# Kernel optimization log

Hardware: AMD Instinct MI355X
Metric: run time of the kernel (lower is better)

Reference implementation:

```python
import jax, jax.numpy as jnp
import numpy as np

B, A, T, D = 8, 50, 256, 128
HEADS, C = 32, 4  # C = D // HEADS
NEG_SLOPE = 0.2   # PyG GATConv default negative_slope


def setup_inputs() -> dict:
    key = jax.random.key(0)
    k1, k2, k3, k4 = jax.random.split(key, 4)
    h = jax.random.normal(k1, (B, A, T, D), dtype=jnp.float32)
    # PyG Linear weight [heads*out, in], applied as x @ W.T
    W = jax.random.normal(k2, (HEADS * C, D), dtype=jnp.float32) * (1.0 / np.sqrt(D))
    att_src = jax.random.normal(k3, (HEADS, C), dtype=jnp.float32) * 0.1
    att_dst = jax.random.normal(k4, (HEADS, C), dtype=jnp.float32) * 0.1
    bias = jnp.zeros((HEADS * C,), dtype=jnp.float32)
    return {"h": h, "W": W, "att_src": att_src, "att_dst": att_dst, "bias": bias}


def reference(h, W, att_src, att_dst, bias):
    # Graph is fully-connected-minus-self over A agents, replicated B*T times.
    # Equivalent dense form: per-destination softmax over all sources j != i.
    Bv, Av, Tv, Dv = h.shape
    x = h.transpose(0, 2, 1, 3).reshape(Bv * Tv, Av, Dv)          # [N, A, D], N = B*T graphs
    x = jnp.einsum('nad,ed->nae', x, W).reshape(Bv * Tv, Av, HEADS, C)  # W x, per head
    a_src = jnp.einsum('nahc,hc->nah', x, att_src)                # alpha_src[j]
    a_dst = jnp.einsum('nahc,hc->nah', x, att_dst)                # alpha_dst[i]
    # edge (j -> i): e_ij = leaky_relu(alpha_src[j] + alpha_dst[i])
    e = a_dst[:, :, None, :] + a_src[:, None, :, :]               # [N, i, j, H]
    e = jnp.where(e > 0, e, NEG_SLOPE * e)
    diag = jnp.eye(Av, dtype=bool)[None, :, :, None]              # no self-loops
    e = jnp.where(diag, -jnp.inf, e)
    alpha = jax.nn.softmax(e, axis=2)                             # scatter-softmax over src per dst
    out = jnp.einsum('nijh,njhc->nihc', alpha, x)                 # scatter-add aggregation
    out = out.reshape(Bv * Tv, Av, HEADS * C) + bias              # concat heads + bias
    return out.reshape(Bv, Tv, Av, HEADS * C).transpose(0, 2, 1, 3)  # (B, A, T, D)
```

## Files before the change

### kernel.cpp

```cpp
#include <hip/hip_runtime.h>
#include <hip/hip_bf16.h>

#define LOG2E 1.4426950408889634f

typedef __attribute__((ext_vector_type(8))) short bf16x8;
typedef __attribute__((ext_vector_type(4))) float f32x4;
typedef __attribute__((ext_vector_type(2))) float v2f;

static __device__ __forceinline__ float fast_exp2(float x) {
    return __builtin_amdgcn_exp2f(x);
}

static __device__ __forceinline__ short bf16bits(float f) {
    __hip_bfloat16 b = __float2bfloat16(f);
    return *reinterpret_cast<short*>(&b);
}

__global__ void wconv(const float* __restrict__ W, short* __restrict__ Wb) {
    const int i = blockIdx.x * 256 + threadIdx.x;
    Wb[i] = bf16bits(W[i]);
}

template<bool PRE>
__global__ __launch_bounds__(256, 3) void gat_fused(
    const float* __restrict__ hsrc,
    const float* __restrict__ W,
    const short* __restrict__ Wb,
    const float* __restrict__ att_src,
    const float* __restrict__ att_dst,
    const float* __restrict__ bias,
    float* __restrict__ out)
{
    constexpr int A = 50, T = 256, D = 128, H = 32;
    constexpr int XSS = 132;
    __shared__ __align__(16) char smem[25600 + A * XSS * 4];
    v2f*   EsFs = (v2f*)smem;
    v2f*   EdFd = (v2f*)(smem + 12800);
    short* hsb  = (short*)smem;
    float* xs   = (float*)(smem + 25600);

    const int n = blockIdx.x;
    const int b = n >> 8;
    const int t = n & 255;
    const int tid = threadIdx.x;

    const float4* hg4 = (const float4*)hsrc;
    for (int idx = tid; idx < 64 * 32; idx += 256) {
        const int a = idx >> 5, k4 = idx & 31;
        short4 pk = {0, 0, 0, 0};
        if (a < A) {
            const float4 hv = hg4[((size_t)(b * A + a) * T + t) * 32 + k4];
            pk.x = bf16bits(hv.x); pk.y = bf16bits(hv.y);
            pk.z = bf16bits(hv.z); pk.w = bf16bits(hv.w);
        }
        const int swz = (k4 >> 1) ^ (a & 7);
        *(short4*)&hsb[a * 128 + swz * 8 + (k4 & 1) * 4] = pk;
    }
    __syncthreads();

    {
        const int wv = tid >> 6;
        const int lane = tid & 63;
        const int lr = lane & 15, lg = lane >> 4;
        const int n0 = wv * 32;
        f32x4 acc[4][2];
        #pragma unroll
        for (int m = 0; m < 4; ++m) {
            acc[m][0] = (f32x4){0.f, 0.f, 0.f, 0.f};
            acc[m][1] = (f32x4){0.f, 0.f, 0.f, 0.f};
        }
        #pragma unroll
        for (int kk = 0; kk < 4; ++kk) {
            bf16x8 bf0, bf1;
            if (PRE) {
                const bf16x8* Wb8 = (const bf16x8*)Wb;
                bf0 = Wb8[(size_t)(n0 + lr) * 16 + kk * 4 + lg];
                bf1 = Wb8[(size_t)(n0 + 16 + lr) * 16 + kk * 4 + lg];
            } else {
                const float4* W4 = (const float4*)W;
                const int kb = kk * 8 + lg * 2;
                const float4 wa = W4[(size_t)(n0 + lr) * 32 + kb];
                const float4 wb = W4[(size_t)(n0 + lr) * 32 + kb + 1];
                const float4 wc = W4[(size_t)(n0 + 16 + lr) * 32 + kb];
                const float4 wd = W4[(size_t)(n0 + 16 + lr) * 32 + kb + 1];
                bf0[0] = bf16bits(wa.x); bf0[1] = bf16bits(wa.y);
                bf0[2] = bf16bits(wa.z); bf0[3] = bf16bits(wa.w);
                bf0[4] = bf16bits(wb.x); bf0[5] = bf16bits(wb.y);
                bf0[6] = bf16bits(wb.z); bf0[7] = bf16bits(wb.w);
                bf1[0] = bf16bits(wc.x); bf1[1] = bf16bits(wc.y);
                bf1[2] = bf16bits(wc.z); bf1[3] = bf16bits(wc.w);
                bf1[4] = bf16bits(wd.x); bf1[5] = bf16bits(wd.y);
                bf1[6] = bf16bits(wd.z); bf1[7] = bf16bits(wd.w);
            }
            #pragma unroll
            for (int m = 0; m < 4; ++m) {
                const int row = m * 16 + lr;
                const int chunk = (kk * 4 + lg) ^ (row & 7);
                const bf16x8 af = *(const bf16x8*)&hsb[row * 128 + chunk * 8];
                acc[m][0] = __builtin_amdgcn_mfma_f32_16x16x32_bf16(af, bf0, acc[m][0], 0, 0, 0);
                acc[m][1] = __builtin_amdgcn_mfma_f32_16x16x32_bf16(af, bf1, acc[m][1], 0, 0, 0);
            }
        }
        #pragma unroll
        for (int m = 0; m < 4; ++m) {
            const int rb = m * 16 + lg * 4;
            #pragma unroll
            for (int nt = 0; nt < 2; ++nt) {
                const int col = n0 + nt * 16 + lr;
                #pragma unroll
                for (int r = 0; r < 4; ++r) {
                    if (rb + r < A) xs[(rb + r) * XSS + col] = acc[m][nt][r];
                }
            }
        }
    }
    __syncthreads();

    for (int idx = tid; idx < A * H; idx += 256) {
        const int hh = idx & 31, a = idx >> 5;
        const float4 xv = *(const float4*)&xs[a * XSS + hh * 4];
        const float4 s4 = ((const float4*)att_src)[hh];
        const float4 d4 = ((const float4*)att_dst)[hh];
        const float asc = LOG2E * fmaf(xv.w, s4.w, fmaf(xv.z, s4.z, fmaf(xv.y, s4.y, xv.x * s4.x)));
        const float ads = LOG2E * fmaf(xv.w, d4.w, fmaf(xv.z, d4.z, fmaf(xv.y, d4.y, xv.x * d4.x)));
        EsFs[idx] = (v2f){fast_exp2(asc), fast_exp2(0.2f * asc)};
        EdFd[idx] = (v2f){fast_exp2(ads), fast_exp2(0.2f * ads)};
    }
    __syncthreads();

    {
        const int hh = tid & 31;
        const int ib = tid >> 5;
        v2f acc01[7], acc23[7], df[7];
        float l[7];
        #pragma unroll
        for (int r = 0; r < 7; ++r) {
            const int i = ib + 8 * r;
            const int ii = (i < A) ? i : (A - 1);
            df[r] = EdFd[ii * H + hh];
            acc01[r] = (v2f){0.f, 0.f};
            acc23[r] = (v2f){0.f, 0.f};
            l[r] = 0.f;
        }
        #pragma unroll 5
        for (int j = 0; j < A; ++j) {
            const v2f sf = EsFs[j * H + hh];
            const float4 xv = *(const float4*)&xs[j * XSS + hh * 4];
            const v2f x01 = (v2f){xv.x, xv.y};
            const v2f x23 = (v2f){xv.z, xv.w};
            #pragma unroll
            for (int r = 0; r < 7; ++r) {
                const v2f pe = df[r] * sf;
                const float p = fmaxf(pe.x, pe.y);
                l[r] += p;
                const v2f pp = (v2f){p, p};
                acc01[r] = __builtin_elementwise_fma(pp, x01, acc01[r]);
                acc23[r] = __builtin_elementwise_fma(pp, x23, acc23[r]);
            }
        }
        const float4 bv = ((const float4*)bias)[hh];
        #pragma unroll
        for (int r = 0; r < 7; ++r) {
            const int i = ib + 8 * r;
            if (i < A) {
                const v2f sf = EsFs[i * H + hh];
                const float4 xv = *(const float4*)&xs[i * XSS + hh * 4];
                const v2f pe = df[r] * sf;
                const float p = fmaxf(pe.x, pe.y);
                const float linv = 1.0f / (l[r] - p);
                float4 o;
                o.x = fmaf(acc01[r].x - p * xv.x, linv, bv.x);
                o.y = fmaf(acc01[r].y - p * xv.y, linv, bv.y);
                o.z = fmaf(acc23[r].x - p * xv.z, linv, bv.z);
                o.w = fmaf(acc23[r].y - p * xv.w, linv, bv.w);
                *(float4*)&out[((size_t)(b * A + i) * T + t) * D + hh * 4] = o;
            }
        }
    }
}

extern "C" void kernel_launch(void* const* d_in, const int* in_sizes, int n_in,
                              void* d_out, int out_size, void* d_ws, size_t ws_size,
                              hipStream_t stream) {
    const float* h       = (const float*)d_in[0];
    const float* W       = (const float*)d_in[1];
    const float* att_src = (const float*)d_in[2];
    const float* att_dst = (const float*)d_in[3];
    const float* bias    = (const float*)d_in[4];
    float* out = (float*)d_out;
    dim3 grid(8 * 256);
    dim3 block(256);
    if (ws_size >= 128 * 128 * sizeof(short)) {
        short* Wb = (short*)d_ws;
        hipLaunchKernelGGL(wconv, dim3(64), block, 0, stream, W, Wb);
        hipLaunchKernelGGL(gat_fused<true>, grid, block, 0, stream,
                           h, W, Wb, att_src, att_dst, bias, out);
    } else {
        hipLaunchKernelGGL(gat_fused<false>, grid, block, 0, stream,
                           h, W, (const short*)nullptr, att_src, att_dst, bias, out);
    }
}
```

Measured before the change: 57.75 us.

## Move attention aggregation onto bf16 MFMA with transposed bf16 projection storage

Replaces the scalar per-thread attention aggregation with a bf16 MFMA. Attention weights are built as the A operand, and the projected features are stored transposed in bf16 in LDS as the B operand. An extra all-ones column computes the softmax denominator inside the same MFMA. Shared memory drops and the launch-bounds occupancy target rises from 3 to 4. The cost is two head phases with extra syncs, rounding of x and the weights to bf16, and a scattered scalar output store of one float per lane.

```diff
diff --git a/kernel.cpp b/kernel.cpp
--- a/kernel.cpp
+++ b/kernel.cpp
@@ -10,11 +10,14 @@
 static __device__ __forceinline__ float fast_exp2(float x) {
     return __builtin_amdgcn_exp2f(x);
 }
-
 static __device__ __forceinline__ short bf16bits(float f) {
     __hip_bfloat16 b = __float2bfloat16(f);
     return *reinterpret_cast<short*>(&b);
 }
+static __device__ __forceinline__ unsigned packbf(float lo, float hi) {
+    return (unsigned)(unsigned short)bf16bits(lo)
+         | ((unsigned)(unsigned short)bf16bits(hi) << 16);
+}
 
 __global__ void wconv(const float* __restrict__ W, short* __restrict__ Wb) {
     const int i = blockIdx.x * 256 + threadIdx.x;
@@ -22,7 +25,7 @@
 }
 
 template<bool PRE>
-__global__ __launch_bounds__(256, 3) void gat_fused(
+__global__ __launch_bounds__(256, 4) void gat_fused(
     const float* __restrict__ hsrc,
     const float* __restrict__ W,
     const short* __restrict__ Wb,
@@ -31,18 +34,20 @@
     const float* __restrict__ bias,
     float* __restrict__ out)
 {
-    constexpr int A = 50, T = 256, D = 128, H = 32;
-    constexpr int XSS = 132;
-    __shared__ __align__(16) char smem[25600 + A * XSS * 4];
-    v2f*   EsFs = (v2f*)smem;
-    v2f*   EdFd = (v2f*)(smem + 12800);
+    constexpr int A = 50, T = 256, D = 128;
+    constexpr int XJ = 72;
+    __shared__ __align__(16) char smem[16384 + 129 * XJ * 2];
+    float* esfs = (float*)smem;
+    float* edfd = (float*)(smem + 8192);
+    short* xsT  = (short*)(smem + 16384);
     short* hsb  = (short*)smem;
-    float* xs   = (float*)(smem + 25600);
 
     const int n = blockIdx.x;
     const int b = n >> 8;
     const int t = n & 255;
     const int tid = threadIdx.x;
+    const int lane = tid & 63, lr = lane & 15, lg = lane >> 4;
+    const int w = tid >> 6;
 
     const float4* hg4 = (const float4*)hsrc;
     for (int idx = tid; idx < 64 * 32; idx += 256) {
@@ -56,13 +61,11 @@
         const int swz = (k4 >> 1) ^ (a & 7);
         *(short4*)&hsb[a * 128 + swz * 8 + (k4 & 1) * 4] = pk;
     }
+    if (tid < 64) xsT[128 * XJ + tid] = (short)0x3F80;
     __syncthreads();
 
     {
-        const int wv = tid >> 6;
-        const int lane = tid & 63;
-        const int lr = lane & 15, lg = lane >> 4;
-        const int n0 = wv * 32;
+        const int n0 = w * 32;
         f32x4 acc[4][2];
         #pragma unroll
         for (int m = 0; m < 4; ++m) {
@@ -103,79 +106,110 @@
         }
         #pragma unroll
         for (int m = 0; m < 4; ++m) {
-            const int rb = m * 16 + lg * 4;
+            const int row0 = m * 16 + lg * 4;
             #pragma unroll
             for (int nt = 0; nt < 2; ++nt) {
                 const int col = n0 + nt * 16 + lr;
+                const unsigned w0 = packbf(acc[m][nt][0], acc[m][nt][1]);
+                const unsigned w1 = packbf(acc[m][nt][2], acc[m][nt][3]);
+                *(uint2*)&xsT[col * XJ + row0] = (uint2){w0, w1};
+            }
+        }
+    }
+    __syncthreads();
+
+    const float4* as4 = (const float4*)att_src;
+    const float4* ad4 = (const float4*)att_dst;
+
+    #pragma unroll 1
+    for (int ph = 0; ph < 2; ++ph) {
+        #pragma unroll
+        for (int p = 0; p < 4; ++p) {
+            const int idx = p * 256 + tid;
+            const int hl = idx >> 6, a = idx & 63;
+            v2f sf = (v2f){0.f, 0.f}, df = (v2f){0.f, 0.f};
+            if (a < A) {
+                const int hg = ph * 16 + hl;
+                const int cb = (hg * 4) * XJ + a;
+                const float x0 = __uint_as_float((unsigned)(unsigned short)xsT[cb] << 16);
+                const float x1 = __uint_as_float((unsigned)(unsigned short)xsT[cb + XJ] << 16);
+                const float x2 = __uint_as_float((unsigned)(unsigned short)xsT[cb + 2 * XJ] << 16);
+                const float x3 = __uint_as_float((unsigned)(unsigned short)xsT[cb + 3 * XJ] << 16);
+                const float4 s4 = as4[hg], d4 = ad4[hg];
+                const float as = LOG2E * fmaf(x3, s4.w, fmaf(x2, s4.z, fmaf(x1, s4.y, x0 * s4.x)));
+                const float ad = LOG2E * fmaf(x3, d4.w, fmaf(x2, d4.z, fmaf(x1, d4.y, x0 * d4.x)));
+                sf = (v2f){fast_exp2(as), fast_exp2(0.2f * as)};
+                df = (v2f){fast_exp2(ad), fast_exp2(0.2f * ad)};
+            }
+            *(v2f*)&esfs[idx * 2] = sf;
+            *(v2f*)&edfd[idx * 2] = df;
+        }
+        __syncthreads();
+
+        #pragma unroll 1
+        for (int u = 0; u < 4; ++u) {
+            const int hl = w * 4 + u;
+            const int hg = ph * 16 + hl;
+            const int colmap = (lr < 4) ? (hg * 4 + lr) : 128;
+            f32x4 acc[4];
+            #pragma unroll
+            for (int m = 0; m < 4; ++m) acc[m] = (f32x4){0.f, 0.f, 0.f, 0.f};
+            #pragma unroll
+            for (int kt = 0; kt < 2; ++kt) {
+                const int k0 = kt * 32;
+                const int j0 = k0 + lg * 8;
+                const float4* ep = (const float4*)&esfs[(hl * 64 + j0) * 2];
+                const float4 e0 = ep[0], e1 = ep[1], e2 = ep[2], e3 = ep[3];
+                union { uint4 q; bf16x8 v; } bfr;
+                bfr.q = *(const uint4*)&xsT[colmap * XJ + j0];
+                #pragma unroll
+                for (int m = 0; m < 4; ++m) {
+                    const int row = m * 16 + lr;
+                    const v2f dd = *(const v2f*)&edfd[(hl * 64 + row) * 2];
+                    float p0 = fmaxf(dd.x * e0.x, dd.y * e0.y);
+                    float p1 = fmaxf(dd.x * e0.z, dd.y * e0.w);
+                    float p2 = fmaxf(dd.x * e1.x, dd.y * e1.y);
+                    float p3 = fmaxf(dd.x * e1.z, dd.y * e1.w);
+                    float p4 = fmaxf(dd.x * e2.x, dd.y * e2.y);
+                    float p5 = fmaxf(dd.x * e2.z, dd.y * e2.w);
+                    float p6 = fmaxf(dd.x * e3.x, dd.y * e3.y);
+                    float p7 = fmaxf(dd.x * e3.z, dd.y * e3.w);
+                    const int dm = m * 16 - k0;
+                    if (dm >= -15 && dm <= 23) {
+                        const int dq = row - j0;
+                        p0 = (dq == 0) ? 0.f : p0;
+                        p1 = (dq == 1) ? 0.f : p1;
+                        p2 = (dq == 2) ? 0.f : p2;
+                        p3 = (dq == 3) ? 0.f : p3;
+                        p4 = (dq == 4) ? 0.f : p4;
+                        p5 = (dq == 5) ? 0.f : p5;
+                        p6 = (dq == 6) ? 0.f : p6;
+                        p7 = (dq == 7) ? 0.f : p7;
+                    }
+                    union { unsigned uu[4]; bf16x8 v; } afr;
+                    afr.uu[0] = packbf(p0, p1);
+                    afr.uu[1] = packbf(p2, p3);
+                    afr.uu[2] = packbf(p4, p5);
+                    afr.uu[3] = packbf(p6, p7);
+                    acc[m] = __builtin_amdgcn_mfma_f32_16x16x32_bf16(afr.v, bfr.v, acc[m], 0, 0, 0);
+                }
+            }
+            const float bv = bias[hg * 4 + (lr & 3)];
+            #pragma unroll
+            for (int m = 0; m < 4; ++m) {
                 #pragma unroll
                 for (int r = 0; r < 4; ++r) {
-                    if (rb + r < A) xs[(rb + r) * XSS + col] = acc[m][nt][r];
+                    const float lsum = __shfl(acc[m][r], (lane & 48) | 4, 64);
+                    const int row = m * 16 + lg * 4 + r;
+                    if (lr < 4 && row < A) {
+                        const float linv = __builtin_amdgcn_rcpf(fmaxf(lsum, 1e-20f));
+                        const float o = fmaf(acc[m][r], linv, bv);
+                        out[((size_t)(b * A + row) * T + t) * D + hg * 4 + lr] = o;
+                    }
                 }
             }
         }
-    }
-    __syncthreads();
-
-    for (int idx = tid; idx < A * H; idx += 256) {
-        const int hh = idx & 31, a = idx >> 5;
-        const float4 xv = *(const float4*)&xs[a * XSS + hh * 4];
-        const float4 s4 = ((const float4*)att_src)[hh];
-        const float4 d4 = ((const float4*)att_dst)[hh];
-        const float asc = LOG2E * fmaf(xv.w, s4.w, fmaf(xv.z, s4.z, fmaf(xv.y, s4.y, xv.x * s4.x)));
-        const float ads = LOG2E * fmaf(xv.w, d4.w, fmaf(xv.z, d4.z, fmaf(xv.y, d4.y, xv.x * d4.x)));
-        EsFs[idx] = (v2f){fast_exp2(asc), fast_exp2(0.2f * asc)};
-        EdFd[idx] = (v2f){fast_exp2(ads), fast_exp2(0.2f * ads)};
-    }
-    __syncthreads();
-
-    {
-        const int hh = tid & 31;
-        const int ib = tid >> 5;
-        v2f acc01[7], acc23[7], df[7];
-        float l[7];
-        #pragma unroll
-        for (int r = 0; r < 7; ++r) {
-            const int i = ib + 8 * r;
-            const int ii = (i < A) ? i : (A - 1);
-            df[r] = EdFd[ii * H + hh];
-            acc01[r] = (v2f){0.f, 0.f};
-            acc23[r] = (v2f){0.f, 0.f};
-            l[r] = 0.f;
-        }
-        #pragma unroll 5
-        for (int j = 0; j < A; ++j) {
-            const v2f sf = EsFs[j * H + hh];
-            const float4 xv = *(const float4*)&xs[j * XSS + hh * 4];
-            const v2f x01 = (v2f){xv.x, xv.y};
-            const v2f x23 = (v2f){xv.z, xv.w};
-            #pragma unroll
-            for (int r = 0; r < 7; ++r) {
-                const v2f pe = df[r] * sf;
-                const float p = fmaxf(pe.x, pe.y);
-                l[r] += p;
-                const v2f pp = (v2f){p, p};
-                acc01[r] = __builtin_elementwise_fma(pp, x01, acc01[r]);
-                acc23[r] = __builtin_elementwise_fma(pp, x23, acc23[r]);
-            }
-        }
-        const float4 bv = ((const float4*)bias)[hh];
-        #pragma unroll
-        for (int r = 0; r < 7; ++r) {
-            const int i = ib + 8 * r;
-            if (i < A) {
-                const v2f sf = EsFs[i * H + hh];
-                const float4 xv = *(const float4*)&xs[i * XSS + hh * 4];
-                const v2f pe = df[r] * sf;
-                const float p = fmaxf(pe.x, pe.y);
-                const float linv = 1.0f / (l[r] - p);
-                float4 o;
-                o.x = fmaf(acc01[r].x - p * xv.x, linv, bv.x);
-                o.y = fmaf(acc01[r].y - p * xv.y, linv, bv.y);
-                o.z = fmaf(acc23[r].x - p * xv.z, linv, bv.z);
-                o.w = fmaf(acc23[r].y - p * xv.w, linv, bv.w);
-                *(float4*)&out[((size_t)(b * A + i) * T + t) * D + hh * 4] = o;
-            }
-        }
+        __syncthreads();
     }
 }
 
```

Result: slower. 93.77 us (+62.4%).

## Split each graph's heads across two blocks to raise occupancy

Applied to the files above, without the earlier changes.

Each graph is now processed by two blocks, each handling 16 of the 32 heads (64 output columns). This halves the shared memory per block and the per-thread register arrays, and launch bounds rise to 6 blocks per CU. The cost is that each block still loads and converts the full h tile to bf16, so global reads of h double and the small GEMM's row tiling is redone per block. A barrier is added before xs is written because xs is no longer separate from the h staging buffer.

```diff
diff --git a/kernel.cpp b/kernel.cpp
--- a/kernel.cpp
+++ b/kernel.cpp
@@ -10,7 +10,6 @@
 static __device__ __forceinline__ float fast_exp2(float x) {
     return __builtin_amdgcn_exp2f(x);
 }
-
 static __device__ __forceinline__ short bf16bits(float f) {
     __hip_bfloat16 b = __float2bfloat16(f);
     return *reinterpret_cast<short*>(&b);
@@ -22,7 +21,7 @@
 }
 
 template<bool PRE>
-__global__ __launch_bounds__(256, 3) void gat_fused(
+__global__ __launch_bounds__(256, 6) void gat_fused(
     const float* __restrict__ hsrc,
     const float* __restrict__ W,
     const short* __restrict__ Wb,
@@ -31,18 +30,22 @@
     const float* __restrict__ bias,
     float* __restrict__ out)
 {
-    constexpr int A = 50, T = 256, D = 128, H = 32;
-    constexpr int XSS = 132;
-    __shared__ __align__(16) char smem[25600 + A * XSS * 4];
-    v2f*   EsFs = (v2f*)smem;
-    v2f*   EdFd = (v2f*)(smem + 12800);
+    constexpr int A = 50, T = 256, D = 128;
+    constexpr int XC = 68;
+    __shared__ __align__(16) char smem[12800 + A * XC * 4];
+    v2f*   tabS = (v2f*)smem;
+    v2f*   tabD = (v2f*)(smem + 6400);
+    float* xs   = (float*)(smem + 12800);
     short* hsb  = (short*)smem;
-    float* xs   = (float*)(smem + 25600);
 
-    const int n = blockIdx.x;
+    const int bid = blockIdx.x;
+    const int n = bid >> 1;
+    const int hp = bid & 1;
     const int b = n >> 8;
     const int t = n & 255;
     const int tid = threadIdx.x;
+    const int lane = tid & 63, lr = lane & 15, lg = lane >> 4;
+    const int wv = tid >> 6;
 
     const float4* hg4 = (const float4*)hsrc;
     for (int idx = tid; idx < 64 * 32; idx += 256) {
@@ -59,97 +62,85 @@
     __syncthreads();
 
     {
-        const int wv = tid >> 6;
-        const int lane = tid & 63;
-        const int lr = lane & 15, lg = lane >> 4;
-        const int n0 = wv * 32;
-        f32x4 acc[4][2];
+        const int rbase = wv * 16;
+        f32x4 acc[4];
         #pragma unroll
-        for (int m = 0; m < 4; ++m) {
-            acc[m][0] = (f32x4){0.f, 0.f, 0.f, 0.f};
-            acc[m][1] = (f32x4){0.f, 0.f, 0.f, 0.f};
-        }
+        for (int nt = 0; nt < 4; ++nt) acc[nt] = (f32x4){0.f, 0.f, 0.f, 0.f};
         #pragma unroll
         for (int kk = 0; kk < 4; ++kk) {
-            bf16x8 bf0, bf1;
-            if (PRE) {
-                const bf16x8* Wb8 = (const bf16x8*)Wb;
-                bf0 = Wb8[(size_t)(n0 + lr) * 16 + kk * 4 + lg];
-                bf1 = Wb8[(size_t)(n0 + 16 + lr) * 16 + kk * 4 + lg];
-            } else {
-                const float4* W4 = (const float4*)W;
-                const int kb = kk * 8 + lg * 2;
-                const float4 wa = W4[(size_t)(n0 + lr) * 32 + kb];
-                const float4 wb = W4[(size_t)(n0 + lr) * 32 + kb + 1];
-                const float4 wc = W4[(size_t)(n0 + 16 + lr) * 32 + kb];
-                const float4 wd = W4[(size_t)(n0 + 16 + lr) * 32 + kb + 1];
-                bf0[0] = bf16bits(wa.x); bf0[1] = bf16bits(wa.y);
-                bf0[2] = bf16bits(wa.z); bf0[3] = bf16bits(wa.w);
-                bf0[4] = bf16bits(wb.x); bf0[5] = bf16bits(wb.y);
-                bf0[6] = bf16bits(wb.z); bf0[7] = bf16bits(wb.w);
-                bf1[0] = bf16bits(wc.x); bf1[1] = bf16bits(wc.y);
-                bf1[2] = bf16bits(wc.z); bf1[3] = bf16bits(wc.w);
-                bf1[4] = bf16bits(wd.x); bf1[5] = bf16bits(wd.y);
-                bf1[6] = bf16bits(wd.z); bf1[7] = bf16bits(wd.w);
-            }
+            const int row = rbase + lr;
+            const int chunk = (kk * 4 + lg) ^ (row & 7);
+            const bf16x8 af = *(const bf16x8*)&hsb[row * 128 + chunk * 8];
             #pragma unroll
-            for (int m = 0; m < 4; ++m) {
-                const int row = m * 16 + lr;
-                const int chunk = (kk * 4 + lg) ^ (row & 7);
-                const bf16x8 af = *(const bf16x8*)&hsb[row * 128 + chunk * 8];
-                acc[m][0] = __builtin_amdgcn_mfma_f32_16x16x32_bf16(af, bf0, acc[m][0], 0, 0, 0);
-                acc[m][1] = __builtin_amdgcn_mfma_f32_16x16x32_bf16(af, bf1, acc[m][1], 0, 0, 0);
+            for (int nt = 0; nt < 4; ++nt) {
+                const int e = hp * 64 + nt * 16 + lr;
+                bf16x8 bf;
+                if (PRE) {
+                    bf = ((const bf16x8*)Wb)[(size_t)e * 16 + kk * 4 + lg];
+                } else {
+                    const float4* W4 = (const float4*)W;
+                    const int kb = kk * 8 + lg * 2;
+                    const float4 wa = W4[(size_t)e * 32 + kb];
+                    const float4 wb = W4[(size_t)e * 32 + kb + 1];
+                    bf[0] = bf16bits(wa.x); bf[1] = bf16bits(wa.y);
+                    bf[2] = bf16bits(wa.z); bf[3] = bf16bits(wa.w);
+                    bf[4] = bf16bits(wb.x); bf[5] = bf16bits(wb.y);
+                    bf[6] = bf16bits(wb.z); bf[7] = bf16bits(wb.w);
+                }
+                acc[nt] = __builtin_amdgcn_mfma_f32_16x16x32_bf16(af, bf, acc[nt], 0, 0, 0);
             }
         }
+        __syncthreads();
         #pragma unroll
-        for (int m = 0; m < 4; ++m) {
-            const int rb = m * 16 + lg * 4;
+        for (int nt = 0; nt < 4; ++nt) {
             #pragma unroll
-            for (int nt = 0; nt < 2; ++nt) {
-                const int col = n0 + nt * 16 + lr;
-                #pragma unroll
-                for (int r = 0; r < 4; ++r) {
-                    if (rb + r < A) xs[(rb + r) * XSS + col] = acc[m][nt][r];
-                }
+            for (int r = 0; r < 4; ++r) {
+                const int row = rbase + lg * 4 + r;
+                if (row < A) xs[row * XC + nt * 16 + lr] = acc[nt][r];
             }
         }
     }
     __syncthreads();
 
-    for (int idx = tid; idx < A * H; idx += 256) {
-        const int hh = idx & 31, a = idx >> 5;
-        const float4 xv = *(const float4*)&xs[a * XSS + hh * 4];
-        const float4 s4 = ((const float4*)att_src)[hh];
-        const float4 d4 = ((const float4*)att_dst)[hh];
-        const float asc = LOG2E * fmaf(xv.w, s4.w, fmaf(xv.z, s4.z, fmaf(xv.y, s4.y, xv.x * s4.x)));
-        const float ads = LOG2E * fmaf(xv.w, d4.w, fmaf(xv.z, d4.z, fmaf(xv.y, d4.y, xv.x * d4.x)));
-        EsFs[idx] = (v2f){fast_exp2(asc), fast_exp2(0.2f * asc)};
-        EdFd[idx] = (v2f){fast_exp2(ads), fast_exp2(0.2f * ads)};
+    for (int p = 0; p < 4; ++p) {
+        const int idx = p * 256 + tid;
+        if (idx < A * 16) {
+            const int a = idx >> 4, hl = idx & 15;
+            const int hg = hp * 16 + hl;
+            const float4 xv = *(const float4*)&xs[a * XC + hl * 4];
+            const float4 s4 = ((const float4*)att_src)[hg];
+            const float4 d4 = ((const float4*)att_dst)[hg];
+            const float asc = LOG2E * fmaf(xv.w, s4.w, fmaf(xv.z, s4.z, fmaf(xv.y, s4.y, xv.x * s4.x)));
+            const float ads = LOG2E * fmaf(xv.w, d4.w, fmaf(xv.z, d4.z, fmaf(xv.y, d4.y, xv.x * d4.x)));
+            tabS[idx] = (v2f){fast_exp2(asc), fast_exp2(0.2f * asc)};
+            tabD[idx] = (v2f){fast_exp2(ads), fast_exp2(0.2f * ads)};
+        }
     }
     __syncthreads();
 
     {
-        const int hh = tid & 31;
-        const int ib = tid >> 5;
-        v2f acc01[7], acc23[7], df[7];
-        float l[7];
+        const int hh = tid & 15;
+        const int ib = tid >> 4;
+        const int hg = hp * 16 + hh;
+        v2f acc01[4], acc23[4], df[4];
+        float l[4];
         #pragma unroll
-        for (int r = 0; r < 7; ++r) {
-            const int i = ib + 8 * r;
+        for (int r = 0; r < 4; ++r) {
+            const int i = ib + 16 * r;
             const int ii = (i < A) ? i : (A - 1);
-            df[r] = EdFd[ii * H + hh];
+            df[r] = tabD[ii * 16 + hh];
             acc01[r] = (v2f){0.f, 0.f};
             acc23[r] = (v2f){0.f, 0.f};
             l[r] = 0.f;
         }
         #pragma unroll 5
         for (int j = 0; j < A; ++j) {
-            const v2f sf = EsFs[j * H + hh];
-            const float4 xv = *(const float4*)&xs[j * XSS + hh * 4];
+            const v2f sf = tabS[j * 16 + hh];
+            const float4 xv = *(const float4*)&xs[j * XC + hh * 4];
             const v2f x01 = (v2f){xv.x, xv.y};
             const v2f x23 = (v2f){xv.z, xv.w};
             #pragma unroll
-            for (int r = 0; r < 7; ++r) {
+            for (int r = 0; r < 4; ++r) {
                 const v2f pe = df[r] * sf;
                 const float p = fmaxf(pe.x, pe.y);
                 l[r] += p;
@@ -158,13 +149,13 @@
                 acc23[r] = __builtin_elementwise_fma(pp, x23, acc23[r]);
             }
         }
-        const float4 bv = ((const float4*)bias)[hh];
+        const float4 bv = ((const float4*)bias)[hg];
         #pragma unroll
-        for (int r = 0; r < 7; ++r) {
-            const int i = ib + 8 * r;
+        for (int r = 0; r < 4; ++r) {
+            const int i = ib + 16 * r;
             if (i < A) {
-                const v2f sf = EsFs[i * H + hh];
-                const float4 xv = *(const float4*)&xs[i * XSS + hh * 4];
+                const v2f sf = tabS[i * 16 + hh];
+                const float4 xv = *(const float4*)&xs[i * XC + hh * 4];
                 const v2f pe = df[r] * sf;
                 const float p = fmaxf(pe.x, pe.y);
                 const float linv = 1.0f / (l[r] - p);
@@ -173,7 +164,7 @@
                 o.y = fmaf(acc01[r].y - p * xv.y, linv, bv.y);
                 o.z = fmaf(acc23[r].x - p * xv.z, linv, bv.z);
                 o.w = fmaf(acc23[r].y - p * xv.w, linv, bv.w);
-                *(float4*)&out[((size_t)(b * A + i) * T + t) * D + hh * 4] = o;
+                *(float4*)&out[((size_t)(b * A + i) * T + t) * D + hg * 4] = o;
             }
         }
     }
@@ -188,7 +179,7 @@
     const float* att_dst = (const float*)d_in[3];
     const float* bias    = (const float*)d_in[4];
     float* out = (float*)d_out;
-    dim3 grid(8 * 256);
+    dim3 grid(8 * 256 * 2);
     dim3 block(256);
     if (ws_size >= 128 * 128 * sizeof(short)) {
         short* Wb = (short*)d_ws;
```

Measured after the change: 79.57 us. 1.38x slower.
